# Kernel optimization log

Hardware: AMD Instinct MI355X
Metric: run time of the kernel (lower is better)

The kernel has to match this reference:

```python
import jax, jax.numpy as jnp
import numpy as np

NUM_TOKENS = 14
DIM = 128
B, N = 8, 128
NUM_ROUNDS = 5


def setup_inputs() -> dict:
    key = jax.random.key(0)
    ks = jax.random.split(key, 10)
    s = 1.0 / np.sqrt(DIM)
    return {
        "tok": jax.random.randint(ks[0], (B, N), 0, NUM_TOKENS),
        "A": jax.random.uniform(ks[1], (B, N, N), dtype=jnp.float32),
        "embed": jax.random.normal(ks[2], (NUM_TOKENS, DIM), dtype=jnp.float32),
        "W1": jax.random.normal(ks[3], (DIM, 2 * DIM), dtype=jnp.float32) * s,
        "b1": jax.random.normal(ks[4], (DIM,), dtype=jnp.float32) * s,
        "W2": jax.random.normal(ks[5], (DIM, DIM), dtype=jnp.float32) * s,
        "b2": jax.random.normal(ks[6], (DIM,), dtype=jnp.float32) * s,
        "Wo1": jax.random.normal(ks[7], (DIM, DIM), dtype=jnp.float32) * s,
        "bo1": jax.random.normal(ks[8], (DIM,), dtype=jnp.float32) * s,
        "Wo2": jax.random.normal(ks[9], (10, DIM), dtype=jnp.float32) * s,
    }


def reference(tok, A, embed, W1, b1, W2, b2, Wo1, bo1, Wo2):
    # Dropout is identity (eval mode / inference reference).
    x = embed[tok]  # [B, N, D]
    d = x.shape[-1]
    # fc1 on concat(x_i, x_j) decomposes into two per-node projections:
    # fc1([x_i, x_j]) = x_i @ W1a^T + x_j @ W1b^T + b1
    W1a, W1b = W1[:, :d], W1[:, d:]
    A_t = jnp.swapaxes(A, 1, 2)  # A.transpose(1, 2)
    for _ in range(NUM_ROUNDS):
        hi = jnp.einsum("bnd,ed->bne", x, W1a)
        hj = jnp.einsum("bnd,ed->bne", x, W1b)
        # pairwise edge MLP: [B, N, N, D]
        h = jax.nn.relu(hi[:, :, None, :] + hj[:, None, :, :] + b1)
        m = jax.nn.relu(jnp.einsum("bijd,ed->bije", h, W2) + b2)
        # mask by transposed adjacency and sum over neighbors j (axis 2)
        msg = jnp.einsum("bij,bije->bie", A_t, m)
        x = x + msg
    def head(z):
        return jax.nn.relu(z @ Wo1.T + bo1) @ Wo2.T
    out = head(x[:, 0, :])                       # [B, 10]
    x_all = head(x.reshape(-1, d)).reshape(x.shape[0], x.shape[1], 10)
    return (out, x_all)
```

## Files before the change

### kernel.cpp

```cpp
#include <hip/hip_runtime.h>
#include <hip/hip_bf16.h>

#define BB 8
#define NN 128
#define DD 128

typedef __attribute__((ext_vector_type(8))) short bf16x8;
typedef __attribute__((ext_vector_type(4))) float floatx4;

__device__ __forceinline__ unsigned short f2bf(float f) {
    unsigned int bits = __float_as_uint(f);
    unsigned int r = bits + 0x7FFFu + ((bits >> 16) & 1u);
    return (unsigned short)(r >> 16);
}

#define WS_X0   0
#define WS_X1   131072
#define WS_W1T  262144
#define WS_W2B  279552
#define WS_CNT  288256

__global__ __launch_bounds__(256) void k_init(const int* __restrict__ tok,
                                              const float* __restrict__ embf,
                                              const float* __restrict__ W1f,
                                              const float* __restrict__ W2f,
                                              float* __restrict__ ws) {
    float* x0 = ws + WS_X0;
    unsigned short* gw1t = (unsigned short*)(ws + WS_W1T);
    unsigned short* gw2b = (unsigned short*)(ws + WS_W2B);
    int* cnt = (int*)(ws + WS_CNT);
    int blk = blockIdx.x, t = threadIdx.x;
    if (blk < 32) {
        int base = blk * 4096;
#pragma unroll
        for (int it = 0; it < 16; ++it) {
            int idx = base + it * 256 + t;
            int r = idx >> 7, d = idx & 127;
            x0[idx] = embf[tok[r] * DD + d];
        }
    } else if (blk < 41) {
        int base = (blk - 32) * 4096;
#pragma unroll
        for (int it = 0; it < 16; ++it) {
            int idx = base + it * 256 + t;
            if (idx < 256 * 136) {
                int e = idx / 136, d = idx - e * 136;
                gw1t[idx] = (d < 128) ? f2bf(W1f[(e & 127) * 256 + (e >> 7) * 128 + d])
                                      : (unsigned short)0;
            }
        }
    } else if (blk < 46) {
        int base = (blk - 41) * 4096;
#pragma unroll
        for (int it = 0; it < 16; ++it) {
            int idx = base + it * 256 + t;
            if (idx < 128 * 136) {
                int e = idx / 136, d = idx - e * 136;
                gw2b[idx] = (d < 128) ? f2bf(W2f[e * 128 + d]) : (unsigned short)0;
            }
        }
    } else if (blk == 46) {
#pragma unroll
        for (int it = 0; it < 4; ++it) cnt[it * 256 + t] = 0;
    }
}

__global__ __launch_bounds__(512, 2) void k_main(const float* __restrict__ Af,
                                                 const float* __restrict__ b1f,
                                                 const float* __restrict__ b2f,
                                                 const float* __restrict__ Wo1f,
                                                 const float* __restrict__ bo1f,
                                                 const float* __restrict__ Wo2f,
                                                 float* __restrict__ ws,
                                                 float* __restrict__ outp) {
    __shared__ __align__(16) unsigned short w1t[256 * 136];
    __shared__ __align__(16) unsigned short w2b[128 * 136];
    __shared__ __align__(16) unsigned short xb[128 * 136];
    __shared__ __align__(16) float red[4][4][128];
    __shared__ __align__(16) float zs[4][128];
    __shared__ float a_s[4][128];
    __shared__ __align__(16) float hja_s[4][128];
    __shared__ float b1s[128], b2s[128];

    float* x0 = ws + WS_X0;
    float* x1 = ws + WS_X1;
    const unsigned short* gw1t = (const unsigned short*)(ws + WS_W1T);
    const unsigned short* gw2b = (const unsigned short*)(ws + WS_W2B);
    int* cnt = (int*)(ws + WS_CNT);

    int blk = blockIdx.x;
    int b = blk >> 5, g = blk & 31, i0 = g * 4;
    int t = threadIdx.x;
    int wave = t >> 6, lane = t & 63;
    int col = lane & 15, quad = lane >> 4;

    {
        const uint4* s1 = (const uint4*)gw1t; uint4* d1 = (uint4*)w1t;
#pragma unroll
        for (int it = 0; it < 9; ++it) { int idx = it * 512 + t; if (idx < 4352) d1[idx] = s1[idx]; }
        const uint4* s2 = (const uint4*)gw2b; uint4* d2 = (uint4*)w2b;
#pragma unroll
        for (int it = 0; it < 5; ++it) { int idx = it * 512 + t; if (idx < 2176) d2[idx] = s2[idx]; }
    }
    if (t < 128) { b1s[t] = b1f[t]; b2s[t] = b2f[t]; }
    a_s[t >> 7][t & 127] = Af[(b * NN + (t & 127)) * NN + i0 + (t >> 7)];

    float xown = x0[(b * NN + i0 + (t >> 7)) * DD + (t & 127)];

    const int myw = i0 >> 4;
    const int qr  = g & 3;

    for (int r = 0; r < 5; ++r) {
        const float* cur = (r & 1) ? x1 : x0;
        float* nxt = (r & 1) ? x0 : x1;
        const float* curb = cur + b * NN * DD;
#pragma unroll
        for (int it = 0; it < 16; ++it) {
            int idx = it * 1024 + t * 2;
            int j = idx >> 7, d = idx & 127;
            unsigned long long v = __hip_atomic_load(
                (unsigned long long*)(curb + j * DD + d),
                __ATOMIC_RELAXED, __HIP_MEMORY_SCOPE_AGENT);
            unsigned int lo = (unsigned int)v, hi2 = (unsigned int)(v >> 32);
            unsigned int packed = (unsigned int)f2bf(__uint_as_float(lo))
                                | ((unsigned int)f2bf(__uint_as_float(hi2)) << 16);
            *reinterpret_cast<unsigned int*>(&xb[j * 136 + d]) = packed;
        }
        __syncthreads();

        bf16x8 af[4];
#pragma unroll
        for (int ks = 0; ks < 4; ++ks)
            af[ks] = *reinterpret_cast<const bf16x8*>(&xb[(wave * 16 + col) * 136 + ks * 32 + quad * 8]);
        floatx4 acc1[16];
#pragma unroll
        for (int nt = 0; nt < 16; ++nt) acc1[nt] = (floatx4){0.f, 0.f, 0.f, 0.f};
#pragma unroll
        for (int nt = 0; nt < 16; ++nt)
#pragma unroll
            for (int ks = 0; ks < 4; ++ks) {
                bf16x8 bfc = *reinterpret_cast<const bf16x8*>(&w1t[(nt * 16 + col) * 136 + ks * 32 + quad * 8]);
                acc1[nt] = __builtin_amdgcn_mfma_f32_16x16x32_bf16(af[ks], bfc, acc1[nt], 0, 0, 0);
            }
        if (wave == myw && quad == qr) {
#pragma unroll
            for (int nt = 0; nt < 8; ++nt) {
                int d = nt * 16 + col;
#pragma unroll
                for (int rr = 0; rr < 4; ++rr) hja_s[rr][d] = acc1[nt][rr];
            }
        }
#pragma unroll
        for (int nt = 8; nt < 16; ++nt) {
            int d = (nt - 8) * 16 + col;
#pragma unroll
            for (int rr = 0; rr < 4; ++rr) {
                int j = wave * 16 + quad * 4 + rr;
                xb[j * 136 + d] = f2bf(acc1[nt][rr] + b1s[d]);
            }
        }
        __syncthreads();

        int we = wave & 1, wj = wave >> 1;
        int ebase = we * 64, jbase = wj * 32;
        bf16x8 bw[4][4];
#pragma unroll
        for (int et = 0; et < 4; ++et)
#pragma unroll
            for (int ks = 0; ks < 4; ++ks)
                bw[et][ks] = *reinterpret_cast<const bf16x8*>(&w2b[(ebase + et * 16 + col) * 136 + ks * 32 + quad * 8]);
#pragma unroll
        for (int ii = 0; ii < 4; ++ii) {
            floatx4 acc2[2][4];
#pragma unroll
            for (int jt = 0; jt < 2; ++jt)
#pragma unroll
                for (int et = 0; et < 4; ++et) acc2[jt][et] = (floatx4){0.f, 0.f, 0.f, 0.f};
#pragma unroll
            for (int jt = 0; jt < 2; ++jt)
#pragma unroll
                for (int ks = 0; ks < 4; ++ks) {
                    int k0 = ks * 32 + quad * 8;
                    union { bf16x8 v; unsigned int u[4]; } Rw, Ho;
                    Rw.v = *reinterpret_cast<const bf16x8*>(&xb[(jbase + jt * 16 + col) * 136 + k0]);
                    const float* hb = &hja_s[ii][k0];
#pragma unroll
                    for (int p = 0; p < 4; ++p) {
                        float f0 = __uint_as_float(Rw.u[p] << 16);
                        float f1 = __uint_as_float(Rw.u[p] & 0xFFFF0000u);
                        f0 = fmaxf(f0 + hb[2 * p], 0.f);
                        f1 = fmaxf(f1 + hb[2 * p + 1], 0.f);
                        Ho.u[p] = (unsigned int)f2bf(f0) | ((unsigned int)f2bf(f1) << 16);
                    }
#pragma unroll
                    for (int et = 0; et < 4; ++et)
                        acc2[jt][et] = __builtin_amdgcn_mfma_f32_16x16x32_bf16(Ho.v, bw[et][ks], acc2[jt][et], 0, 0, 0);
                }
#pragma unroll
            for (int et = 0; et < 4; ++et) {
                int e = ebase + et * 16 + col;
                float be = b2s[e];
                float s = 0.f;
#pragma unroll
                for (int jt = 0; jt < 2; ++jt) {
                    int j0 = jbase + jt * 16 + quad * 4;
#pragma unroll
                    for (int rr = 0; rr < 4; ++rr)
                        s += a_s[ii][j0 + rr] * fmaxf(acc2[jt][et][rr] + be, 0.f);
                }
                s += __shfl_xor(s, 16, 64);
                s += __shfl_xor(s, 32, 64);
                if (quad == 0) red[wj][ii][e] = s;
            }
        }
        __syncthreads();
        {
            int ii = t >> 7, e = t & 127;
            float msg = red[0][ii][e] + red[1][ii][e] + red[2][ii][e] + red[3][ii][e];
            xown += msg;
            if (r < 4) {
                __hip_atomic_store((float*)(nxt + (b * NN + i0 + ii) * DD + e), xown,
                                   __ATOMIC_RELAXED, __HIP_MEMORY_SCOPE_AGENT);
            } else {
                zs[ii][e] = xown;
            }
        }
        if (r < 4) {
            __atomic_signal_fence(__ATOMIC_SEQ_CST);
            __builtin_amdgcn_s_waitcnt(0);
            __syncthreads();
            if (t == 0) {
                int* myc = cnt + (b * 4 + r) * 32;
                __hip_atomic_fetch_add(myc, 1, __ATOMIC_RELAXED, __HIP_MEMORY_SCOPE_AGENT);
                while (__hip_atomic_load(myc, __ATOMIC_RELAXED, __HIP_MEMORY_SCOPE_AGENT) < 32)
                    __builtin_amdgcn_s_sleep(8);
            }
            __syncthreads();
        } else {
            __syncthreads();
        }
    }

    float* wo1s = (float*)w1t;
#pragma unroll
    for (int it = 0; it < 32; ++it) {
        int idx = it * 512 + t;
        int e = idx >> 7, d = idx & 127;
        wo1s[e * 136 + d] = Wo1f[idx];
    }
    __syncthreads();
    {
        int ii = t >> 7, e = t & 127;
        float acc = 0.f;
#pragma unroll
        for (int d4 = 0; d4 < 32; ++d4) {
            float4 w = *reinterpret_cast<const float4*>(&wo1s[e * 136 + d4 * 4]);
            float4 z = *reinterpret_cast<const float4*>(&zs[ii][d4 * 4]);
            acc += w.x * z.x + w.y * z.y + w.z * z.z + w.w * z.w;
        }
        ((float*)red)[ii * 128 + e] = fmaxf(acc + bo1f[e], 0.f);
    }
    __syncthreads();
    if (t < 40) {
        int ii = t / 10, o = t - ii * 10;
        const float* rsrow = (const float*)red + ii * 128;
        float s = 0.f;
#pragma unroll
        for (int e = 0; e < 128; ++e) s += rsrow[e] * Wo2f[o * DD + e];
        int row = b * NN + i0 + ii;
        outp[80 + row * 10 + o] = s;
        if (i0 + ii == 0) outp[b * 10 + o] = s;
    }
}

extern "C" void kernel_launch(void* const* d_in, const int* in_sizes, int n_in,
                              void* d_out, int out_size, void* d_ws, size_t ws_size,
                              hipStream_t stream) {
    const int*   tok  = (const int*)d_in[0];
    const float* Af   = (const float*)d_in[1];
    const float* embf = (const float*)d_in[2];
    const float* W1f  = (const float*)d_in[3];
    const float* b1f  = (const float*)d_in[4];
    const float* W2f  = (const float*)d_in[5];
    const float* b2f  = (const float*)d_in[6];
    const float* Wo1f = (const float*)d_in[7];
    const float* bo1f = (const float*)d_in[8];
    const float* Wo2f = (const float*)d_in[9];

    float* ws  = (float*)d_ws;
    float* out = (float*)d_out;

    k_init<<<48, 256, 0, stream>>>(tok, embf, W1f, W2f, ws);
    k_main<<<256, 512, 0, stream>>>(Af, b1f, b2f, Wo1f, bo1f, Wo2f, ws, out);
}
```

Measured before the change: 168.8 us.

## Exchange node state as bf16, skip redundant hi GEMM, hoist hj unpack, use hw cvt

Node features shared between blocks are now stored in global memory as packed bf16 rather than fp32, with inline-asm cache-bypassing dwordx4 loads, which halves the exchange traffic each round. The first-projection GEMM for the hi half now runs only in the wave that owns this block's rows. The hj bf16 unpack is hoisted out of the ii loop, the adds use packed f32 instructions, and bf16 conversion uses the hardware cvt_pk instruction. Other changes: block-to-batch mapping is interleaved, the spin-wait sleep is shortened, and the head weight loads are vectorized. The fp32 residual is kept per block, but each round's state is broadcast in bf16; the pre-change code already converted it to bf16 on load, so precision is unchanged.

```diff
diff --git a/kernel.cpp b/kernel.cpp
--- a/kernel.cpp
+++ b/kernel.cpp
@@ -7,6 +7,7 @@
 
 typedef __attribute__((ext_vector_type(8))) short bf16x8;
 typedef __attribute__((ext_vector_type(4))) float floatx4;
+typedef __attribute__((ext_vector_type(2))) float floatx2;
 
 __device__ __forceinline__ unsigned short f2bf(float f) {
     unsigned int bits = __float_as_uint(f);
@@ -14,32 +15,45 @@
     return (unsigned short)(r >> 16);
 }
 
-#define WS_X0   0
-#define WS_X1   131072
-#define WS_W1T  262144
-#define WS_W2B  279552
-#define WS_CNT  288256
+__device__ __forceinline__ unsigned short f2bf_hw(float f) {
+    unsigned int r;
+    asm("v_cvt_pk_bf16_f32 %0, %1, %2" : "=v"(r) : "v"(f), "v"(f));
+    return (unsigned short)r;
+}
+
+__device__ __forceinline__ unsigned int f2bf_pk(float lo, float hi) {
+    unsigned int r;
+    asm("v_cvt_pk_bf16_f32 %0, %1, %2" : "=v"(r) : "v"(lo), "v"(hi));
+    return r;
+}
+
+#define WS_X16A 0
+#define WS_X16B 65536
+#define WS_W1T  131072
+#define WS_W2B  148480
+#define WS_CNT  157184
 
 __global__ __launch_bounds__(256) void k_init(const int* __restrict__ tok,
                                               const float* __restrict__ embf,
                                               const float* __restrict__ W1f,
                                               const float* __restrict__ W2f,
                                               float* __restrict__ ws) {
-    float* x0 = ws + WS_X0;
+    unsigned int* x16 = (unsigned int*)(ws + WS_X16A);
     unsigned short* gw1t = (unsigned short*)(ws + WS_W1T);
     unsigned short* gw2b = (unsigned short*)(ws + WS_W2B);
     int* cnt = (int*)(ws + WS_CNT);
     int blk = blockIdx.x, t = threadIdx.x;
-    if (blk < 32) {
+    if (blk < 16) {
         int base = blk * 4096;
 #pragma unroll
         for (int it = 0; it < 16; ++it) {
-            int idx = base + it * 256 + t;
-            int r = idx >> 7, d = idx & 127;
-            x0[idx] = embf[tok[r] * DD + d];
-        }
-    } else if (blk < 41) {
-        int base = (blk - 32) * 4096;
+            int w = base + it * 256 + t;
+            int r = w >> 6, d2 = (w & 63) * 2;
+            const float* er = embf + tok[r] * DD;
+            x16[w] = (unsigned int)f2bf(er[d2]) | ((unsigned int)f2bf(er[d2 + 1]) << 16);
+        }
+    } else if (blk < 25) {
+        int base = (blk - 16) * 4096;
 #pragma unroll
         for (int it = 0; it < 16; ++it) {
             int idx = base + it * 256 + t;
@@ -49,8 +63,8 @@
                                       : (unsigned short)0;
             }
         }
-    } else if (blk < 46) {
-        int base = (blk - 41) * 4096;
+    } else if (blk < 30) {
+        int base = (blk - 25) * 4096;
 #pragma unroll
         for (int it = 0; it < 16; ++it) {
             int idx = base + it * 256 + t;
@@ -59,13 +73,15 @@
                 gw2b[idx] = (d < 128) ? f2bf(W2f[e * 128 + d]) : (unsigned short)0;
             }
         }
-    } else if (blk == 46) {
+    } else if (blk == 30) {
 #pragma unroll
         for (int it = 0; it < 4; ++it) cnt[it * 256 + t] = 0;
     }
 }
 
-__global__ __launch_bounds__(512, 2) void k_main(const float* __restrict__ Af,
+__global__ __launch_bounds__(512, 2) void k_main(const int* __restrict__ tokp,
+                                                 const float* __restrict__ embf,
+                                                 const float* __restrict__ Af,
                                                  const float* __restrict__ b1f,
                                                  const float* __restrict__ b2f,
                                                  const float* __restrict__ Wo1f,
@@ -82,14 +98,12 @@
     __shared__ __align__(16) float hja_s[4][128];
     __shared__ float b1s[128], b2s[128];
 
-    float* x0 = ws + WS_X0;
-    float* x1 = ws + WS_X1;
     const unsigned short* gw1t = (const unsigned short*)(ws + WS_W1T);
     const unsigned short* gw2b = (const unsigned short*)(ws + WS_W2B);
     int* cnt = (int*)(ws + WS_CNT);
 
     int blk = blockIdx.x;
-    int b = blk >> 5, g = blk & 31, i0 = g * 4;
+    int b = blk & 7, g = blk >> 3, i0 = g * 4;
     int t = threadIdx.x;
     int wave = t >> 6, lane = t & 63;
     int col = lane & 15, quad = lane >> 4;
@@ -105,28 +119,38 @@
     if (t < 128) { b1s[t] = b1f[t]; b2s[t] = b2f[t]; }
     a_s[t >> 7][t & 127] = Af[(b * NN + (t & 127)) * NN + i0 + (t >> 7)];
 
-    float xown = x0[(b * NN + i0 + (t >> 7)) * DD + (t & 127)];
-
-    const int myw = i0 >> 4;
+    float xown = embf[tokp[b * NN + i0 + (t >> 7)] * DD + (t & 127)];
+
+    const int myw = g >> 2;
     const int qr  = g & 3;
 
+    __syncthreads();
+
     for (int r = 0; r < 5; ++r) {
-        const float* cur = (r & 1) ? x1 : x0;
-        float* nxt = (r & 1) ? x0 : x1;
-        const float* curb = cur + b * NN * DD;
-#pragma unroll
-        for (int it = 0; it < 16; ++it) {
-            int idx = it * 1024 + t * 2;
-            int j = idx >> 7, d = idx & 127;
-            unsigned long long v = __hip_atomic_load(
-                (unsigned long long*)(curb + j * DD + d),
-                __ATOMIC_RELAXED, __HIP_MEMORY_SCOPE_AGENT);
-            unsigned int lo = (unsigned int)v, hi2 = (unsigned int)(v >> 32);
-            unsigned int packed = (unsigned int)f2bf(__uint_as_float(lo))
-                                | ((unsigned int)f2bf(__uint_as_float(hi2)) << 16);
-            *reinterpret_cast<unsigned int*>(&xb[j * 136 + d]) = packed;
-        }
-        __syncthreads();
+        const unsigned short* cur16 = (const unsigned short*)(ws + ((r & 1) ? WS_X16B : WS_X16A));
+        unsigned short* nxt16 = (unsigned short*)(ws + ((r & 1) ? WS_X16A : WS_X16B));
+
+        {
+            const bf16x8* gp = reinterpret_cast<const bf16x8*>(
+                cur16 + (size_t)(b * NN + wave * 16) * DD);
+            bf16x8 v0, v1, v2, v3;
+            const bf16x8* pl = gp + lane;
+            asm volatile(
+                "global_load_dwordx4 %0, %4, off sc0 sc1\n\t"
+                "global_load_dwordx4 %1, %4, off offset:1024 sc0 sc1\n\t"
+                "global_load_dwordx4 %2, %4, off offset:2048 sc0 sc1\n\t"
+                "global_load_dwordx4 %3, %4, off offset:3072 sc0 sc1\n\t"
+                "s_waitcnt vmcnt(0)"
+                : "=&v"(v0), "=&v"(v1), "=&v"(v2), "=&v"(v3)
+                : "v"(pl)
+                : "memory");
+            int r16 = lane >> 4, c8 = (lane & 15) * 8;
+            *reinterpret_cast<bf16x8*>(&xb[(wave * 16 + r16     ) * 136 + c8]) = v0;
+            *reinterpret_cast<bf16x8*>(&xb[(wave * 16 + r16 + 4 ) * 136 + c8]) = v1;
+            *reinterpret_cast<bf16x8*>(&xb[(wave * 16 + r16 + 8 ) * 136 + c8]) = v2;
+            *reinterpret_cast<bf16x8*>(&xb[(wave * 16 + r16 + 12) * 136 + c8]) = v3;
+            __threadfence_block();
+        }
 
         bf16x8 af[4];
 #pragma unroll
@@ -134,20 +158,31 @@
             af[ks] = *reinterpret_cast<const bf16x8*>(&xb[(wave * 16 + col) * 136 + ks * 32 + quad * 8]);
         floatx4 acc1[16];
 #pragma unroll
-        for (int nt = 0; nt < 16; ++nt) acc1[nt] = (floatx4){0.f, 0.f, 0.f, 0.f};
-#pragma unroll
-        for (int nt = 0; nt < 16; ++nt)
+        for (int nt = 8; nt < 16; ++nt) acc1[nt] = (floatx4){0.f, 0.f, 0.f, 0.f};
+#pragma unroll
+        for (int nt = 8; nt < 16; ++nt)
 #pragma unroll
             for (int ks = 0; ks < 4; ++ks) {
                 bf16x8 bfc = *reinterpret_cast<const bf16x8*>(&w1t[(nt * 16 + col) * 136 + ks * 32 + quad * 8]);
                 acc1[nt] = __builtin_amdgcn_mfma_f32_16x16x32_bf16(af[ks], bfc, acc1[nt], 0, 0, 0);
             }
-        if (wave == myw && quad == qr) {
-#pragma unroll
-            for (int nt = 0; nt < 8; ++nt) {
-                int d = nt * 16 + col;
-#pragma unroll
-                for (int rr = 0; rr < 4; ++rr) hja_s[rr][d] = acc1[nt][rr];
+        if (wave == myw) {
+#pragma unroll
+            for (int nt = 0; nt < 8; ++nt) acc1[nt] = (floatx4){0.f, 0.f, 0.f, 0.f};
+#pragma unroll
+            for (int nt = 0; nt < 8; ++nt)
+#pragma unroll
+                for (int ks = 0; ks < 4; ++ks) {
+                    bf16x8 bfc = *reinterpret_cast<const bf16x8*>(&w1t[(nt * 16 + col) * 136 + ks * 32 + quad * 8]);
+                    acc1[nt] = __builtin_amdgcn_mfma_f32_16x16x32_bf16(af[ks], bfc, acc1[nt], 0, 0, 0);
+                }
+            if (quad == qr) {
+#pragma unroll
+                for (int nt = 0; nt < 8; ++nt) {
+                    int d = nt * 16 + col;
+#pragma unroll
+                    for (int rr = 0; rr < 4; ++rr) hja_s[rr][d] = acc1[nt][rr];
+                }
             }
         }
 #pragma unroll
@@ -156,7 +191,7 @@
 #pragma unroll
             for (int rr = 0; rr < 4; ++rr) {
                 int j = wave * 16 + quad * 4 + rr;
-                xb[j * 136 + d] = f2bf(acc1[nt][rr] + b1s[d]);
+                xb[j * 136 + d] = f2bf_hw(acc1[nt][rr] + b1s[d]);
             }
         }
         __syncthreads();
@@ -169,6 +204,23 @@
 #pragma unroll
             for (int ks = 0; ks < 4; ++ks)
                 bw[et][ks] = *reinterpret_cast<const bf16x8*>(&w2b[(ebase + et * 16 + col) * 136 + ks * 32 + quad * 8]);
+
+        floatx2 hjc[2][4][4];
+#pragma unroll
+        for (int jt = 0; jt < 2; ++jt)
+#pragma unroll
+            for (int ks = 0; ks < 4; ++ks) {
+                union { bf16x8 v; unsigned int u[4]; } Rw;
+                Rw.v = *reinterpret_cast<const bf16x8*>(&xb[(jbase + jt * 16 + col) * 136 + ks * 32 + quad * 8]);
+#pragma unroll
+                for (int p = 0; p < 4; ++p) {
+                    floatx2 h2;
+                    h2.x = __uint_as_float(Rw.u[p] << 16);
+                    h2.y = __uint_as_float(Rw.u[p] & 0xFFFF0000u);
+                    hjc[jt][ks][p] = h2;
+                }
+            }
+
 #pragma unroll
         for (int ii = 0; ii < 4; ++ii) {
             floatx4 acc2[2][4];
@@ -177,25 +229,28 @@
 #pragma unroll
                 for (int et = 0; et < 4; ++et) acc2[jt][et] = (floatx4){0.f, 0.f, 0.f, 0.f};
 #pragma unroll
-            for (int jt = 0; jt < 2; ++jt)
-#pragma unroll
-                for (int ks = 0; ks < 4; ++ks) {
-                    int k0 = ks * 32 + quad * 8;
-                    union { bf16x8 v; unsigned int u[4]; } Rw, Ho;
-                    Rw.v = *reinterpret_cast<const bf16x8*>(&xb[(jbase + jt * 16 + col) * 136 + k0]);
-                    const float* hb = &hja_s[ii][k0];
+            for (int ks = 0; ks < 4; ++ks) {
+                int k0 = ks * 32 + quad * 8;
+                floatx2 ha[4];
+#pragma unroll
+                for (int p = 0; p < 4; ++p)
+                    ha[p] = *reinterpret_cast<const floatx2*>(&hja_s[ii][k0 + 2 * p]);
+#pragma unroll
+                for (int jt = 0; jt < 2; ++jt) {
+                    union { bf16x8 v; unsigned int u[4]; } Ho;
 #pragma unroll
                     for (int p = 0; p < 4; ++p) {
-                        float f0 = __uint_as_float(Rw.u[p] << 16);
-                        float f1 = __uint_as_float(Rw.u[p] & 0xFFFF0000u);
-                        f0 = fmaxf(f0 + hb[2 * p], 0.f);
-                        f1 = fmaxf(f1 + hb[2 * p + 1], 0.f);
-                        Ho.u[p] = (unsigned int)f2bf(f0) | ((unsigned int)f2bf(f1) << 16);
+                        floatx2 s2;
+                        asm("v_pk_add_f32 %0, %1, %2" : "=v"(s2) : "v"(hjc[jt][ks][p]), "v"(ha[p]));
+                        float f0 = fmaxf(s2.x, 0.f);
+                        float f1 = fmaxf(s2.y, 0.f);
+                        Ho.u[p] = f2bf_pk(f0, f1);
                     }
 #pragma unroll
                     for (int et = 0; et < 4; ++et)
                         acc2[jt][et] = __builtin_amdgcn_mfma_f32_16x16x32_bf16(Ho.v, bw[et][ks], acc2[jt][et], 0, 0, 0);
                 }
+            }
 #pragma unroll
             for (int et = 0; et < 4; ++et) {
                 int e = ebase + et * 16 + col;
@@ -219,8 +274,12 @@
             float msg = red[0][ii][e] + red[1][ii][e] + red[2][ii][e] + red[3][ii][e];
             xown += msg;
             if (r < 4) {
-                __hip_atomic_store((float*)(nxt + (b * NN + i0 + ii) * DD + e), xown,
-                                   __ATOMIC_RELAXED, __HIP_MEMORY_SCOPE_AGENT);
+                float po = __shfl_xor(xown, 1, 64);
+                if ((e & 1) == 0) {
+                    unsigned int pk = f2bf_pk(xown, po);
+                    unsigned int* dst = (unsigned int*)nxt16 + (((b * NN + i0 + ii) * DD + e) >> 1);
+                    __hip_atomic_store(dst, pk, __ATOMIC_RELAXED, __HIP_MEMORY_SCOPE_AGENT);
+                }
             } else {
                 zs[ii][e] = xown;
             }
@@ -233,7 +292,7 @@
                 int* myc = cnt + (b * 4 + r) * 32;
                 __hip_atomic_fetch_add(myc, 1, __ATOMIC_RELAXED, __HIP_MEMORY_SCOPE_AGENT);
                 while (__hip_atomic_load(myc, __ATOMIC_RELAXED, __HIP_MEMORY_SCOPE_AGENT) < 32)
-                    __builtin_amdgcn_s_sleep(8);
+                    __builtin_amdgcn_s_sleep(1);
             }
             __syncthreads();
         } else {
@@ -243,10 +302,11 @@
 
     float* wo1s = (float*)w1t;
 #pragma unroll
-    for (int it = 0; it < 32; ++it) {
-        int idx = it * 512 + t;
-        int e = idx >> 7, d = idx & 127;
-        wo1s[e * 136 + d] = Wo1f[idx];
+    for (int it = 0; it < 8; ++it) {
+        int idx4 = it * 512 + t;
+        int e = idx4 >> 5, d4 = idx4 & 31;
+        float4 wv = reinterpret_cast<const float4*>(Wo1f)[idx4];
+        *reinterpret_cast<float4*>(&wo1s[e * 136 + d4 * 4]) = wv;
     }
     __syncthreads();
     {
@@ -264,9 +324,14 @@
     if (t < 40) {
         int ii = t / 10, o = t - ii * 10;
         const float* rsrow = (const float*)red + ii * 128;
+        const float4* w2r = reinterpret_cast<const float4*>(Wo2f + o * DD);
         float s = 0.f;
 #pragma unroll
-        for (int e = 0; e < 128; ++e) s += rsrow[e] * Wo2f[o * DD + e];
+        for (int e4 = 0; e4 < 32; ++e4) {
+            float4 rv = *reinterpret_cast<const float4*>(&rsrow[e4 * 4]);
+            float4 wv = w2r[e4];
+            s += rv.x * wv.x + rv.y * wv.y + rv.z * wv.z + rv.w * wv.w;
+        }
         int row = b * NN + i0 + ii;
         outp[80 + row * 10 + o] = s;
         if (i0 + ii == 0) outp[b * 10 + o] = s;
@@ -290,6 +355,6 @@
     float* ws  = (float*)d_ws;
     float* out = (float*)d_out;
 
-    k_init<<<48, 256, 0, stream>>>(tok, embf, W1f, W2f, ws);
-    k_main<<<256, 512, 0, stream>>>(Af, b1f, b2f, Wo1f, bo1f, Wo2f, ws, out);
-}
+    k_init<<<31, 256, 0, stream>>>(tok, embf, W1f, W2f, ws);
+    k_main<<<256, 512, 0, stream>>>(tok, embf, Af, b1f, b2f, Wo1f, bo1f, Wo2f, ws, out);
+}
```

After: 144.8 us. -14.2%, faster.
